# Kernel tuning notes

Hardware: AMD Instinct MI355X
Metric: run time of the kernel (lower is better)

Reference implementation:

```python
import jax, jax.numpy as jnp
import numpy as np

D_MODEL = 512
D_INNER = 1024   # expand * d_model
D_STATE = 16
DT_RANK = 32     # ceil(d_model / 16)
D_CONV = 4
BATCH = 4
SEQLEN = 2304
DILATIONS = (1, 2, 4)


def _dw(x, w, pad, dil=1):
    # depthwise 1D conv: x (B,C,L), w (C,1,K)
    return jax.lax.conv_general_dilated(
        x, w, window_strides=(1,), padding=[pad], rhs_dilation=(dil,),
        dimension_numbers=('NCH', 'OIH', 'NCH'), feature_group_count=x.shape[1])


def setup_inputs() -> dict:
    key = jax.random.key(0)
    ks = iter(jax.random.split(key, 32))
    nrm = lambda shape, s=0.02: jax.random.normal(next(ks), shape, jnp.float32) * s
    std = DT_RANK ** -0.5
    return dict(
        hidden_states=jax.random.normal(next(ks), (BATCH, SEQLEN, D_MODEL), jnp.float32),
        in_proj_w=nrm((5 * D_INNER, D_MODEL)),
        conv1d_w=nrm((D_INNER, 1, D_CONV), 0.2),
        conv1d_b=jnp.zeros((D_INNER,), jnp.float32),
        x_proj_w=nrm((DT_RANK + 2 * D_STATE, D_INNER)),
        dt_proj_w=jax.random.uniform(next(ks), (D_INNER, DT_RANK), jnp.float32, -std, std),
        dt_proj_b=jax.random.uniform(next(ks), (D_INNER,), jnp.float32, -5.0, -1.0),
        A_log=jnp.log(jnp.broadcast_to(jnp.arange(1, D_STATE + 1, dtype=jnp.float32), (D_INNER, D_STATE))),
        D=jnp.ones((D_INNER,), jnp.float32),
        out_proj_w=nrm((D_MODEL, 3 * D_INNER)),
        cb_local_w=nrm((D_MODEL, 1, 3), 0.2), cb_local_b=jnp.zeros((D_MODEL,), jnp.float32),
        cb_global_w=nrm((D_MODEL, 1, 1), 0.2), cb_global_b=jnp.zeros((D_MODEL,), jnp.float32),
        cb_pre_w=nrm((3, D_MODEL, 1, 1), 0.2), cb_pre_b=jnp.zeros((3, D_MODEL), jnp.float32),
        cb_dil_w=nrm((3, D_MODEL, 1, 3), 0.2), cb_dil_b=jnp.zeros((3, D_MODEL), jnp.float32),
        cb_ln_g=jnp.ones((4 * D_MODEL,), jnp.float32), cb_ln_b=jnp.zeros((4 * D_MODEL,), jnp.float32),
        cb_fuse_w=nrm((2 * D_MODEL, 4 * D_MODEL, 1)), cb_fuse_b=jnp.zeros((2 * D_MODEL,), jnp.float32),
    )


def reference(hidden_states, in_proj_w, conv1d_w, conv1d_b, x_proj_w, dt_proj_w,
              dt_proj_b, A_log, D, out_proj_w, cb_local_w, cb_local_b,
              cb_global_w, cb_global_b, cb_pre_w, cb_pre_b, cb_dil_w, cb_dil_b,
              cb_ln_g, cb_ln_b, cb_fuse_w, cb_fuse_b):
    B, L, dm = hidden_states.shape
    d_inner = D.shape[0]
    d_state = A_log.shape[1]
    dt_rank = dt_proj_w.shape[1]

    # in_proj -> (B, 5*d_inner, L)
    xz = jnp.einsum('ed,bld->bel', in_proj_w, hidden_states)
    xz_f = xz[:, :2 * d_inner]
    xz_b = xz[:, 2 * d_inner:4 * d_inner]
    xz_1 = xz[:, 4 * d_inner:]
    # bidirectional: stack forward and time-flipped backward along batch
    xzc = jnp.concatenate([xz_f, jnp.flip(xz_b, -1)], axis=0)  # (2B, 2*d_inner, L)
    x, z = xzc[:, :d_inner], xzc[:, d_inner:]

    # causal depthwise conv + SiLU
    kc = conv1d_w.shape[-1]
    x = _dw(x, conv1d_w, (kc - 1, 0)) + conv1d_b[None, :, None]
    x = jax.nn.silu(x)

    # x_proj -> dt, B, C
    x_dbl = jnp.einsum('kd,bdl->bkl', x_proj_w, x)
    dt = x_dbl[:, :dt_rank]
    Bm = x_dbl[:, dt_rank:dt_rank + d_state]
    Cm = x_dbl[:, dt_rank + d_state:]
    delta = jax.nn.softplus(jnp.einsum('dr,brl->bdl', dt_proj_w, dt) + dt_proj_b[None, :, None])
    A = -jnp.exp(A_log)  # (d, n)

    # selective scan over time
    delta_l = jnp.moveaxis(delta, 2, 0)  # (L, 2B, d)
    u_l = jnp.moveaxis(x, 2, 0)          # (L, 2B, d)
    B_l = jnp.moveaxis(Bm, 2, 0)         # (L, 2B, n)
    C_l = jnp.moveaxis(Cm, 2, 0)         # (L, 2B, n)

    def step(h, t):
        dl, ul, Bl, Cl = t
        dA = jnp.exp(dl[..., None] * A)                    # (2B, d, n)
        h = dA * h + (dl * ul)[..., None] * Bl[:, None, :]
        y = jnp.einsum('bdn,bn->bd', h, Cl)
        return h, y

    h0 = jnp.zeros((x.shape[0], d_inner, d_state), x.dtype)
    _, ys = jax.lax.scan(step, h0, (delta_l, u_l, B_l, C_l))
    y = jnp.moveaxis(ys, 0, 2)  # (2B, d, L)
    y = y + D[None, :, None] * x
    y = y * jax.nn.silu(z)
    out = jnp.concatenate([y[:B], jnp.flip(y[B:], -1)], axis=1)  # (B, 2*d_inner, L)

    # ConvBranch on xz_1 (2*dm channels -> split into xa, xc of dm each)
    xa, xc = xz_1[:, :dm], xz_1[:, dm:]
    local = jax.nn.gelu(_dw(xc, cb_local_w, (1, 1)) + cb_local_b[None, :, None], approximate=False)
    phi = jax.nn.relu(cb_global_w[:, 0, 0][None, :] * xc.mean(-1) + cb_global_b[None, :])  # (B, dm)
    feats = []
    for i, d in enumerate(DILATIONS):
        xp = cb_pre_w[i, :, 0, 0][None, :, None] * xa + cb_pre_b[i][None, :, None]
        feats.append(_dw(xp, cb_dil_w[i], (d, d), dil=d) + cb_dil_b[i][None, :, None])
    cat = jnp.concatenate(feats + [phi[:, :, None] * local], axis=1)  # (B, 4*dm, L)
    c = cat.transpose(0, 2, 1)
    mu = c.mean(-1, keepdims=True)
    var = c.var(-1, keepdims=True)
    c = (c - mu) / jnp.sqrt(var + 1e-5) * cb_ln_g + cb_ln_b
    cat = c.transpose(0, 2, 1)
    out_c = jnp.einsum('oc,bcl->bol', cb_fuse_w[:, :, 0], cat) + cb_fuse_b[None, :, None]  # (B, 2*d_inner... = d_inner? no: 2*dm, L)

    out_f = jnp.concatenate([out, out_c], axis=1)  # (B, 3*d_inner, L)
    return jnp.einsum('md,bdl->blm', out_proj_w, out_f)  # (B, L, d_model)
```

## Files before the change

### kernel.cpp

```cpp
#include <hip/hip_runtime.h>
#include <math.h>

#define L 2304
#define NB 4
#define NCH 36
#define STILE 64
#define SPAD 68
#define DLU_PAD 130

typedef __attribute__((ext_vector_type(8))) short short8v;
typedef __attribute__((ext_vector_type(4))) float f32x4;

__device__ inline unsigned short f2bf(float x) {
    unsigned u = __float_as_uint(x);
    return (unsigned short)((u + 0x7fffu + ((u >> 16) & 1u)) >> 16);
}
__device__ inline void split1(float x, unsigned short& h, unsigned short& l) {
    h = f2bf(x);
    float hf = __uint_as_float((unsigned)h << 16);
    l = f2bf(x - hf);
}

__device__ __forceinline__ void gload16(const unsigned short* g, unsigned short* l)
{
    __builtin_amdgcn_global_load_lds(
        (const __attribute__((address_space(1))) unsigned int*)g,
        (__attribute__((address_space(3))) unsigned int*)l, 16, 0, 0);
}

__device__ inline float row_reduce16(float v) {
    v += __int_as_float(__builtin_amdgcn_update_dpp(0, __float_as_int(v), 0xB1, 0xF, 0xF, true));
    v += __int_as_float(__builtin_amdgcn_update_dpp(0, __float_as_int(v), 0x4E, 0xF, 0xF, true));
    v += __int_as_float(__builtin_amdgcn_update_dpp(0, __float_as_int(v), 0x124, 0xF, 0xF, true));
    v += __int_as_float(__builtin_amdgcn_update_dpp(0, __float_as_int(v), 0x128, 0xF, 0xF, true));
    return v;
}

__global__ __launch_bounds__(256) void split_kernel(
    const float* __restrict__ src, unsigned short* __restrict__ hi,
    unsigned short* __restrict__ lo, int n)
{
    int i = (blockIdx.x * 256 + threadIdx.x) * 4;
    if (i >= n) return;
    float4 v = *(const float4*)(src + i);
    unsigned short h0, h1, h2, h3, l0, l1, l2, l3;
    split1(v.x, h0, l0); split1(v.y, h1, l1);
    split1(v.z, h2, l2); split1(v.w, h3, l3);
    ushort4 hv; hv.x = h0; hv.y = h1; hv.z = h2; hv.w = h3;
    ushort4 lv; lv.x = l0; lv.y = l1; lv.z = l2; lv.w = l3;
    *(ushort4*)(hi + i) = hv;
    *(ushort4*)(lo + i) = lv;
}

__global__ __launch_bounds__(256) void split_t_kernel(
    const float* __restrict__ src, unsigned short* __restrict__ hiT,
    unsigned short* __restrict__ loT, int C)
{
    __shared__ float tile[64][65];
    const int l0 = blockIdx.x * 64, c0 = blockIdx.y * 64;
    const int li = threadIdx.x & 63, q = threadIdx.x >> 6;
    for (int cc = q; cc < 64; cc += 4)
        tile[cc][li] = src[(long)(c0 + cc) * L + l0 + li];
    __syncthreads();
    const int ci = threadIdx.x & 63;
    for (int ll = q; ll < 64; ll += 4) {
        float x = tile[ci][ll];
        unsigned short h, l;
        split1(x, h, l);
        long o = (long)(l0 + ll) * C + c0 + ci;
        hiT[o] = h;
        loT[o] = l;
    }
}

__global__ __launch_bounds__(256) void gemm_mfma(
    const unsigned short* __restrict__ Ahi, const unsigned short* __restrict__ Alo, int lda,
    const unsigned short* __restrict__ Bhi, const unsigned short* __restrict__ Blo, int ldb,
    float* __restrict__ C, long cms, long cns, int K, int act,
    const float* __restrict__ emu, const float* __restrict__ ers,
    const float* __restrict__ es1, const float* __restrict__ es2)
{
    __shared__ unsigned short Ah[128 * 32], Al[128 * 32], Bh[128 * 32], Bl[128 * 32];
    const int tid = threadIdx.x;
    const int lane = tid & 63, wave = tid >> 6;
    const int wm = (wave >> 1) * 64, wn = (wave & 1) * 64;
    const int m0 = blockIdx.x * 128, n0 = blockIdx.y * 128;
    const int rowS = tid >> 2;
    const int cS = ((tid & 3) ^ ((tid >> 3) & 3)) * 8;
    const unsigned short* gAh0 = Ahi + (long)(m0 + rowS) * lda + cS;
    const unsigned short* gAl0 = Alo + (long)(m0 + rowS) * lda + cS;
    const unsigned short* gBh0 = Bhi + (long)(n0 + rowS) * ldb + cS;
    const unsigned short* gBl0 = Blo + (long)(n0 + rowS) * ldb + cS;
    const long a64 = (long)64 * lda, b64 = (long)64 * ldb;
    unsigned short* lAh0 = Ah + tid * 8;  unsigned short* lAh1 = Ah + 2048 + tid * 8;
    unsigned short* lAl0 = Al + tid * 8;  unsigned short* lAl1 = Al + 2048 + tid * 8;
    unsigned short* lBh0 = Bh + tid * 8;  unsigned short* lBh1 = Bh + 2048 + tid * 8;
    unsigned short* lBl0 = Bl + tid * 8;  unsigned short* lBl1 = Bl + 2048 + tid * 8;
    const int fr = lane & 15;
    const int chq = (((lane >> 4) ^ ((fr >> 1) & 3)) << 3);

    f32x4 acc[4][4];
#pragma unroll
    for (int i = 0; i < 4; ++i)
#pragma unroll
        for (int j = 0; j < 4; ++j) acc[i][j] = (f32x4){0.f, 0.f, 0.f, 0.f};

    for (int k0 = 0; k0 < K; k0 += 32) {
        gload16(gAh0 + k0, lAh0); gload16(gAh0 + a64 + k0, lAh1);
        gload16(gAl0 + k0, lAl0); gload16(gAl0 + a64 + k0, lAl1);
        gload16(gBh0 + k0, lBh0); gload16(gBh0 + b64 + k0, lBh1);
        gload16(gBl0 + k0, lBl0); gload16(gBl0 + b64 + k0, lBl1);
        __syncthreads();
        short8v bhf[4], blf[4];
#pragma unroll
        for (int nf = 0; nf < 4; ++nf) {
            bhf[nf] = *(const short8v*)&Bh[(wn + nf * 16 + fr) * 32 + chq];
            blf[nf] = *(const short8v*)&Bl[(wn + nf * 16 + fr) * 32 + chq];
        }
#pragma unroll
        for (int mf = 0; mf < 4; ++mf) {
            short8v ah = *(const short8v*)&Ah[(wm + mf * 16 + fr) * 32 + chq];
            short8v al = *(const short8v*)&Al[(wm + mf * 16 + fr) * 32 + chq];
#pragma unroll
            for (int nf = 0; nf < 4; ++nf) {
                acc[mf][nf] = __builtin_amdgcn_mfma_f32_16x16x32_bf16(ah, bhf[nf], acc[mf][nf], 0, 0, 0);
                acc[mf][nf] = __builtin_amdgcn_mfma_f32_16x16x32_bf16(ah, blf[nf], acc[mf][nf], 0, 0, 0);
                acc[mf][nf] = __builtin_amdgcn_mfma_f32_16x16x32_bf16(al, bhf[nf], acc[mf][nf], 0, 0, 0);
            }
        }
        __syncthreads();
    }
    const int rb = (lane >> 4) * 4;
#pragma unroll
    for (int mf = 0; mf < 4; ++mf) {
#pragma unroll
        for (int nf = 0; nf < 4; ++nf) {
            int n = n0 + wn + nf * 16 + fr;
            int mb = m0 + wm + mf * 16 + rb;
            if (cms == 1) {
                float4 r;
                r.x = acc[mf][nf][0]; r.y = acc[mf][nf][1];
                r.z = acc[mf][nf][2]; r.w = acc[mf][nf][3];
                *(float4*)(C + (long)n * cns + mb) = r;
            } else {
#pragma unroll
                for (int r = 0; r < 4; ++r) {
                    int m = mb + r;
                    float v = acc[mf][nf][r];
                    if (act == 2) v = (v - emu[n] * es1[m]) * ers[n] + es2[m];
                    C[(long)m * cms + n] = v;
                }
            }
        }
    }
}

__global__ __launch_bounds__(256) void gemm_mfma128sk(
    const unsigned short* __restrict__ Ahi, const unsigned short* __restrict__ Alo, int lda,
    const unsigned short* __restrict__ Bhi, const unsigned short* __restrict__ Blo, int ldb,
    float* __restrict__ P, int KS, int Mstride)
{
    __shared__ unsigned short Ah[128 * 32], Al[128 * 32], Bh[128 * 32], Bl[128 * 32];
    const int tid = threadIdx.x;
    const int lane = tid & 63, wave = tid >> 6;
    const int wm = (wave >> 1) * 64, wn = (wave & 1) * 64;
    const int nwg = gridDim.x * gridDim.y * gridDim.z;
    const int bid = blockIdx.x + gridDim.x * (blockIdx.y + gridDim.y * blockIdx.z);
    const int cpx = nwg >> 3;
    const int swz = (bid & 7) * cpx + (bid >> 3);
    const int bx = swz % gridDim.x;
    const int rest = swz / gridDim.x;
    const int by = rest % gridDim.y;
    const int sl = rest / gridDim.y;
    const int m0 = bx * 128, n0 = by * 128;
    const int kbase = sl * KS;
    const int rowS = tid >> 2;
    const int cS = ((tid & 3) ^ ((tid >> 3) & 3)) * 8;
    const unsigned short* gAh0 = Ahi + (long)(m0 + rowS) * lda + kbase + cS;
    const unsigned short* gAl0 = Alo + (long)(m0 + rowS) * lda + kbase + cS;
    const unsigned short* gBh0 = Bhi + (long)(n0 + rowS) * ldb + kbase + cS;
    const unsigned short* gBl0 = Blo + (long)(n0 + rowS) * ldb + kbase + cS;
    const long a64 = (long)64 * lda, b64 = (long)64 * ldb;
    unsigned short* lAh0 = Ah + tid * 8;  unsigned short* lAh1 = Ah + 2048 + tid * 8;
    unsigned short* lAl0 = Al + tid * 8;  unsigned short* lAl1 = Al + 2048 + tid * 8;
    unsigned short* lBh0 = Bh + tid * 8;  unsigned short* lBh1 = Bh + 2048 + tid * 8;
    unsigned short* lBl0 = Bl + tid * 8;  unsigned short* lBl1 = Bl + 2048 + tid * 8;
    const int fr = lane & 15;
    const int chq = (((lane >> 4) ^ ((fr >> 1) & 3)) << 3);

    f32x4 acc[4][4];
#pragma unroll
    for (int i = 0; i < 4; ++i)
#pragma unroll
        for (int j = 0; j < 4; ++j) acc[i][j] = (f32x4){0.f, 0.f, 0.f, 0.f};

    for (int k0 = 0; k0 < KS; k0 += 32) {
        gload16(gAh0 + k0, lAh0); gload16(gAh0 + a64 + k0, lAh1);
        gload16(gAl0 + k0, lAl0); gload16(gAl0 + a64 + k0, lAl1);
        gload16(gBh0 + k0, lBh0); gload16(gBh0 + b64 + k0, lBh1);
        gload16(gBl0 + k0, lBl0); gload16(gBl0 + b64 + k0, lBl1);
        __syncthreads();
        short8v bhf[4], blf[4];
#pragma unroll
        for (int nf = 0; nf < 4; ++nf) {
            bhf[nf] = *(const short8v*)&Bh[(wn + nf * 16 + fr) * 32 + chq];
            blf[nf] = *(const short8v*)&Bl[(wn + nf * 16 + fr) * 32 + chq];
        }
#pragma unroll
        for (int mf = 0; mf < 4; ++mf) {
            short8v ah = *(const short8v*)&Ah[(wm + mf * 16 + fr) * 32 + chq];
            short8v al = *(const short8v*)&Al[(wm + mf * 16 + fr) * 32 + chq];
#pragma unroll
            for (int nf = 0; nf < 4; ++nf) {
                acc[mf][nf] = __builtin_amdgcn_mfma_f32_16x16x32_bf16(ah, bhf[nf], acc[mf][nf], 0, 0, 0);
                acc[mf][nf] = __builtin_amdgcn_mfma_f32_16x16x32_bf16(ah, blf[nf], acc[mf][nf], 0, 0, 0);
                acc[mf][nf] = __builtin_amdgcn_mfma_f32_16x16x32_bf16(al, bhf[nf], acc[mf][nf], 0, 0, 0);
            }
        }
        __syncthreads();
    }
    const int rb = (lane >> 4) * 4;
    float* Pp = P + (long)sl * Mstride * L;
#pragma unroll
    for (int mf = 0; mf < 4; ++mf) {
#pragma unroll
        for (int nf = 0; nf < 4; ++nf) {
            int n = n0 + wn + nf * 16 + fr;
            int mb = m0 + wm + mf * 16 + rb;
            float4 r;
            r.x = acc[mf][nf][0]; r.y = acc[mf][nf][1];
            r.z = acc[mf][nf][2]; r.w = acc[mf][nf][3];
            *(float4*)(Pp + (long)n * Mstride + mb) = r;
        }
    }
}

__global__ __launch_bounds__(256) void out_reduce(
    const float* __restrict__ P, float* __restrict__ out)
{
    const long E = (long)512 * L;
    long i = ((long)blockIdx.x * 256 + threadIdx.x) * 4;
    float4 r = *(const float4*)(P + i);
#pragma unroll
    for (int s = 1; s < 8; ++s) {
        float4 a = *(const float4*)(P + (long)s * E + i);
        r.x += a.x; r.y += a.y; r.z += a.z; r.w += a.w;
    }
    *(float4*)(out + i) = r;
}

__global__ __launch_bounds__(256) void fuse_reduce(
    const float* __restrict__ P,
    const float* __restrict__ emu, const float* __restrict__ ers,
    const float* __restrict__ es1, const float* __restrict__ es2,
    float* __restrict__ out)
{
    __shared__ float tile[64][65];
    const int m0 = blockIdx.x * 64, n0 = blockIdx.y * 64;
    const int li = threadIdx.x & 63, q = threadIdx.x >> 6;
    const long E = (long)1024 * L;
    for (int nn = q; nn < 64; nn += 4) {
        long base = (long)(n0 + nn) * 1024 + m0 + li;
        tile[nn][li] = (P[base] + P[E + base]) + (P[2 * E + base] + P[3 * E + base]);
    }
    __syncthreads();
    for (int mm = q; mm < 64; mm += 4) {
        int m = m0 + mm, n = n0 + li;
        float v = tile[li][mm];
        v = (v - emu[n] * es1[m]) * ers[n] + es2[m];
        out[(long)m * L + n] = v;
    }
}

__global__ __launch_bounds__(256) void gemm_f32(
    const float* __restrict__ A, int lda,
    const float* __restrict__ B, long ldb, int b_nk, long bbs,
    float* __restrict__ C, long cms, long cns, long cbs,
    int M, int N, int K,
    const float* __restrict__ bias, int act,
    const float* __restrict__ emu, const float* __restrict__ ers,
    const float* __restrict__ es1, const float* __restrict__ es2)
{
    __shared__ float As[16][65];
    __shared__ float Bs[16][65];
    const int tid = threadIdx.x;
    const int tx = tid & 15, ty = tid >> 4;
    const int m0 = blockIdx.x * 64, n0 = blockIdx.y * 64;
    const int bz = blockIdx.z;
    const float* Bb = B + (long)bz * bbs;
    float acc[4][4];
#pragma unroll
    for (int i = 0; i < 4; ++i)
#pragma unroll
        for (int j = 0; j < 4; ++j) acc[i][j] = 0.f;

    for (int k0 = 0; k0 < K; k0 += 16) {
        {
            int m = tid >> 2, kq = (tid & 3) << 2;
            float4 v = *(const float4*)(A + (long)(m0 + m) * lda + (k0 + kq));
            As[kq + 0][m] = v.x; As[kq + 1][m] = v.y; As[kq + 2][m] = v.z; As[kq + 3][m] = v.w;
        }
        if (b_nk) {
            int n = tid >> 2, kq = (tid & 3) << 2;
            float4 v = *(const float4*)(Bb + (long)(n0 + n) * ldb + (k0 + kq));
            Bs[kq + 0][n] = v.x; Bs[kq + 1][n] = v.y; Bs[kq + 2][n] = v.z; Bs[kq + 3][n] = v.w;
        } else {
            int k = tid >> 4, nq = (tid & 15) << 2;
            float4 v = *(const float4*)(Bb + (long)(k0 + k) * ldb + (n0 + nq));
            Bs[k][nq + 0] = v.x; Bs[k][nq + 1] = v.y; Bs[k][nq + 2] = v.z; Bs[k][nq + 3] = v.w;
        }
        __syncthreads();
#pragma unroll
        for (int kk = 0; kk < 16; ++kk) {
            float a[4], b[4];
#pragma unroll
            for (int i = 0; i < 4; ++i) a[i] = As[kk][ty * 4 + i];
#pragma unroll
            for (int j = 0; j < 4; ++j) b[j] = Bs[kk][tx * 4 + j];
#pragma unroll
            for (int i = 0; i < 4; ++i)
#pragma unroll
                for (int j = 0; j < 4; ++j) acc[i][j] = fmaf(a[i], b[j], acc[i][j]);
        }
        __syncthreads();
    }
#pragma unroll
    for (int i = 0; i < 4; ++i) {
        int m = m0 + ty * 4 + i;
        float bs = bias ? bias[m] : 0.f;
        float s1 = es1 ? es1[m] : 0.f;
        float s2 = es2 ? es2[m] : 0.f;
#pragma unroll
        for (int j = 0; j < 4; ++j) {
            int n = n0 + tx * 4 + j;
            float v = acc[i][j] + bs;
            if (act == 1) v = (v > 20.f) ? v : log1pf(expf(v));
            else if (act == 2) {
                float mu = emu[n];
                float rs = ers[n];
                v = (v - mu * s1) * rs + s2;
            }
            C[(long)bz * cbs + (long)m * cms + (long)n * cns] = v;
        }
    }
}

__global__ __launch_bounds__(256) void xproj_partial(
    const float* __restrict__ W, const float* __restrict__ xconv,
    float* __restrict__ P)
{
    __shared__ float As[16][65];
    __shared__ float Bs[16][65];
    const int tid = threadIdx.x;
    const int tx = tid & 15, ty = tid >> 4;
    const int n0 = blockIdx.x * 64;
    const int dir = blockIdx.y, sl = blockIdx.z;
    const float* A = W + sl * 256;
    const float* B = xconv + ((long)dir * 1024 + sl * 256) * L;
    float* Pp = P + ((long)sl * 2 + dir) * 64 * L;
    float acc[4][4];
#pragma unroll
    for (int i = 0; i < 4; ++i)
#pragma unroll
        for (int j = 0; j < 4; ++j) acc[i][j] = 0.f;

    for (int k0 = 0; k0 < 256; k0 += 16) {
        {
            int m = tid >> 2, kq = (tid & 3) << 2;
            float4 v = *(const float4*)(A + (long)m * 1024 + (k0 + kq));
            As[kq + 0][m] = v.x; As[kq + 1][m] = v.y; As[kq + 2][m] = v.z; As[kq + 3][m] = v.w;
        }
        {
            int k = tid >> 4, nq = (tid & 15) << 2;
            float4 v = *(const float4*)(B + (long)(k0 + k) * L + (n0 + nq));
            Bs[k][nq + 0] = v.x; Bs[k][nq + 1] = v.y; Bs[k][nq + 2] = v.z; Bs[k][nq + 3] = v.w;
        }
        __syncthreads();
#pragma unroll
        for (int kk = 0; kk < 16; ++kk) {
            float a[4], b[4];
#pragma unroll
            for (int i = 0; i < 4; ++i) a[i] = As[kk][ty * 4 + i];
#pragma unroll
            for (int j = 0; j < 4; ++j) b[j] = Bs[kk][tx * 4 + j];
#pragma unroll
            for (int i = 0; i < 4; ++i)
#pragma unroll
                for (int j = 0; j < 4; ++j) acc[i][j] = fmaf(a[i], b[j], acc[i][j]);
        }
        __syncthreads();
    }
#pragma unroll
    for (int i = 0; i < 4; ++i) {
        int m = ty * 4 + i;
        float4 r;
        r.x = acc[i][0]; r.y = acc[i][1]; r.z = acc[i][2]; r.w = acc[i][3];
        *(float4*)(Pp + (long)m * L + n0 + tx * 4) = r;
    }
}

__global__ __launch_bounds__(256) void xproj_reduce(
    const float* __restrict__ P, float* __restrict__ xdbl)
{
    const long E = (long)2 * 64 * L;
    long i = ((long)blockIdx.x * 256 + threadIdx.x) * 4;
    float4 a = *(const float4*)(P + i);
    float4 b = *(const float4*)(P + E + i);
    float4 c = *(const float4*)(P + 2 * E + i);
    float4 d = *(const float4*)(P + 3 * E + i);
    float4 r;
    r.x = (a.x + b.x) + (c.x + d.x);
    r.y = (a.y + b.y) + (c.y + d.y);
    r.z = (a.z + b.z) + (c.z + d.z);
    r.w = (a.w + b.w) + (c.w + d.w);
    *(float4*)(xdbl + i) = r;
}

__global__ __launch_bounds__(256) void mamba_conv_kernel(
    const float* __restrict__ xz_b, const float* __restrict__ w,
    const float* __restrict__ bias, float* __restrict__ xout)
{
    long idx = (long)blockIdx.x * 256 + threadIdx.x;
    int l = (int)(idx % L);
    long r = idx / L;
    int d = (int)(r % 1024);
    int dir = (int)(r / 1024);
    const float* src = xz_b + ((dir ? 2048 : 0) + (long)d) * L;
    float acc = bias[d];
#pragma unroll
    for (int j = 0; j < 4; ++j) {
        int t = l - 3 + j;
        if (t >= 0) {
            float v = dir ? src[L - 1 - t] : src[t];
            acc = fmaf(w[d * 4 + j], v, acc);
        }
    }
    xout[idx] = acc / (1.f + expf(-acc));
}

__global__ __launch_bounds__(256) void scan_pass1(
    const float* __restrict__ delta_b, const float* __restrict__ xconv_b,
    const float* __restrict__ xdbl_b, const float* __restrict__ A_log,
    float* __restrict__ hend, float* __restrict__ pAb)
{
    __shared__ float s_dlu[16][DLU_PAD];
    __shared__ float s_B[16][SPAD];
    const int tid = threadIdx.x;
    const int dir = blockIdx.y, ch = blockIdx.z;
    const int n = tid & 15, dloc = tid >> 4;
    const int d0 = blockIdx.x * 16;
    const int d = d0 + dloc;
    const int t0 = ch * STILE;
    const float Adn = -expf(A_log[d * 16 + n]);
    const float* dl_p = delta_b + ((long)dir * 1024 + d0) * L;
    const float* u_p  = xconv_b + ((long)dir * 1024 + d0) * L;
    const float* B_p  = xdbl_b + ((long)dir * 64 + 32) * L;
    const int lch = tid >> 4, lq = tid & 15;
    {
        float4 a = *(const float4*)(dl_p + (long)lch * L + t0 + lq * 4);
        float4 b = *(const float4*)(u_p + (long)lch * L + t0 + lq * 4);
        float4 w0; w0.x = a.x; w0.y = b.x; w0.z = a.y; w0.w = b.y;
        float4 w1; w1.x = a.z; w1.y = b.z; w1.z = a.w; w1.w = b.w;
        *(float4*)&s_dlu[lch][lq * 8] = w0;
        *(float4*)&s_dlu[lch][lq * 8 + 4] = w1;
        float4 v = *(const float4*)(B_p + (long)lch * L + t0 + lq * 4);
        *(float4*)&s_B[lch][lq * 4] = v;
    }
    __syncthreads();
    float h = 0.f, p = 1.f;
#pragma unroll 4
    for (int tt = 0; tt < STILE; ++tt) {
        float2 dlu = *(const float2*)&s_dlu[dloc][tt * 2];
        float Bv = s_B[n][tt];
        float dA = __expf(dlu.x * Adn);
        h = fmaf(dA, h, dlu.x * dlu.y * Bv);
        p *= dA;
    }
    long sidx = (((long)dir * NCH + ch) * 1024 + d) * 16 + n;
    hend[sidx] = h;
    pAb[sidx] = p;
}

__global__ __launch_bounds__(256) void scan_fix(
    const float* __restrict__ hend, const float* __restrict__ pAb,
    float* __restrict__ hin)
{
    int tid = blockIdx.x * 256 + threadIdx.x;
    int dir = tid >> 14;
    int rest = tid & 16383;
    float h = 0.f;
#pragma unroll
    for (int c = 0; c < NCH; ++c) {
        long idx = (((long)dir * NCH + c) << 14) + rest;
        hin[idx] = h;
        h = hend[idx] + pAb[idx] * h;
    }
}

__global__ __launch_bounds__(256) void scan_pass2(
    const float* __restrict__ delta_b, const float* __restrict__ xconv_b,
    const float* __restrict__ xdbl_b, const float* __restrict__ xz_b,
    const float* __restrict__ A_log, const float* __restrict__ Dvec,
    const float* __restrict__ hin, float* __restrict__ out_fb)
{
    __shared__ float s_dlu[16][DLU_PAD];
    __shared__ float s_BC[16][DLU_PAD];
    const int tid = threadIdx.x;
    const int dir = blockIdx.y, ch = blockIdx.z;
    const int n = tid & 15, dloc = tid >> 4;
    const int d0 = blockIdx.x * 16;
    const int d = d0 + dloc;
    const int t0 = ch * STILE;
    const int opos0 = dir ? (L - STILE - t0) : t0;
    const float Adn = -expf(A_log[d * 16 + n]);
    const float Dd = Dvec[d];
    const float* dl_p = delta_b + ((long)dir * 1024 + d0) * L;
    const float* u_p  = xconv_b + ((long)dir * 1024 + d0) * L;
    const float* B_p  = xdbl_b + ((long)dir * 64 + 32) * L;
    const float* C_p  = xdbl_b + ((long)dir * 64 + 48) * L;
    const float* z_p  = xz_b + ((dir ? 3072 : 1024) + (long)d0) * L;
    float* o_p = out_fb + ((dir ? 1024 : 0) + (long)d0) * L;
    const int lch = tid >> 4, lq = tid & 15;
    {
        float4 a = *(const float4*)(dl_p + (long)lch * L + t0 + lq * 4);
        float4 b = *(const float4*)(u_p + (long)lch * L + t0 + lq * 4);
        float4 w0; w0.x = a.x; w0.y = b.x; w0.z = a.y; w0.w = b.y;
        float4 w1; w1.x = a.z; w1.y = b.z; w1.z = a.w; w1.w = b.w;
        *(float4*)&s_dlu[lch][lq * 8] = w0;
        *(float4*)&s_dlu[lch][lq * 8 + 4] = w1;
        float4 c = *(const float4*)(B_p + (long)lch * L + t0 + lq * 4);
        float4 e = *(const float4*)(C_p + (long)lch * L + t0 + lq * 4);
        float4 x0; x0.x = c.x; x0.y = e.x; x0.z = c.y; x0.w = e.y;
        float4 x1; x1.x = c.z; x1.y = e.z; x1.z = c.w; x1.w = e.w;
        *(float4*)&s_BC[lch][lq * 8] = x0;
        *(float4*)&s_BC[lch][lq * 8 + 4] = x1;
    }
    __syncthreads();
    float h = hin[(((long)dir * NCH + ch) * 1024 + d) * 16 + n];
#pragma unroll 4
    for (int tt = 0; tt < STILE; ++tt) {
        float2 dlu = *(const float2*)&s_dlu[dloc][tt * 2];
        float2 bc = *(const float2*)&s_BC[n][tt * 2];
        float dA = __expf(dlu.x * Adn);
        h = fmaf(dA, h, dlu.x * dlu.y * bc.x);
        float y = row_reduce16(h * bc.y);
        if (n == 0) s_dlu[dloc][tt * 2] = y + Dd * dlu.y;
    }
    {
        float* po = o_p + (long)lch * L + opos0;
        const float* pz = z_p + (long)lch * L + opos0;
        int oo = lq * 4;
        float4 zv = *(const float4*)(pz + oo);
        float y0 = s_dlu[lch][(dir ? 63 - oo : oo) * 2];
        float y1 = s_dlu[lch][(dir ? 62 - oo : oo + 1) * 2];
        float y2 = s_dlu[lch][(dir ? 61 - oo : oo + 2) * 2];
        float y3 = s_dlu[lch][(dir ? 60 - oo : oo + 3) * 2];
        float4 r;
        r.x = y0 * (zv.x / (1.f + __expf(-zv.x)));
        r.y = y1 * (zv.y / (1.f + __expf(-zv.y)));
        r.z = y2 * (zv.z / (1.f + __expf(-zv.z)));
        r.w = y3 * (zv.w / (1.f + __expf(-zv.w)));
        *(float4*)(po + oo) = r;
    }
}

__global__ __launch_bounds__(256) void mean_phi_kernel(
    const float* __restrict__ xz_b, const float* __restrict__ gw,
    const float* __restrict__ gb, float* __restrict__ phi_b)
{
    int c = blockIdx.x;
    const float* src = xz_b + (4608 + (long)c) * L;
    float s = 0.f;
    for (int l = threadIdx.x; l < L; l += 256) s += src[l];
    __shared__ float red[256];
    red[threadIdx.x] = s;
    __syncthreads();
    for (int st = 128; st > 0; st >>= 1) {
        if (threadIdx.x < st) red[threadIdx.x] += red[threadIdx.x + st];
        __syncthreads();
    }
    if (threadIdx.x == 0) {
        float m = red[0] / (float)L;
        phi_b[c] = fmaxf(gw[c] * m + gb[c], 0.f);
    }
}

__global__ __launch_bounds__(256) void cat_build_kernel(
    const float* __restrict__ xz_b,
    const float* __restrict__ lw, const float* __restrict__ lb,
    const float* __restrict__ pw, const float* __restrict__ pb,
    const float* __restrict__ dw, const float* __restrict__ db,
    const float* __restrict__ phi_b, float* __restrict__ cat_b)
{
    long idx = (long)blockIdx.x * 256 + threadIdx.x;
    int l = (int)(idx % L);
    int cc = (int)(idx / L);
    float val;
    if (cc < 1536) {
        int i = cc >> 9, c = cc & 511, dil = 1 << i;
        const float* xa = xz_b + (4096 + (long)c) * L;
        float pwv = pw[i * 512 + c], pbv = pb[i * 512 + c];
        const float* w = dw + ((long)i * 512 + c) * 3;
        float acc = db[i * 512 + c];
#pragma unroll
        for (int k = 0; k < 3; ++k) {
            int t = l + (k - 1) * dil;
            if (t >= 0 && t < L) acc += (pwv * xa[t] + pbv) * w[k];
        }
        val = acc;
    } else {
        int c = cc & 511;
        const float* xc = xz_b + (4608 + (long)c) * L;
        float acc = lb[c];
#pragma unroll
        for (int k = 0; k < 3; ++k) {
            int t = l - 1 + k;
            if (t >= 0 && t < L) acc += xc[t] * lw[c * 3 + k];
        }
        float g = 0.5f * acc * (1.f + erff(acc * 0.70710678118f));
        val = phi_b[c] * g;
    }
    cat_b[idx] = val;
}

__global__ __launch_bounds__(256) void ln_partial_kernel(
    const float* __restrict__ cat_b, float* __restrict__ ps, float* __restrict__ pq)
{
    int l = blockIdx.x * 256 + threadIdx.x;
    int g = blockIdx.y;
    const float* p = cat_b + (long)g * 64 * L + l;
    float s = 0.f, q = 0.f;
#pragma unroll 8
    for (int c = 0; c < 64; ++c) {
        float v = p[(long)c * L];
        s += v;
        q = fmaf(v, v, q);
    }
    ps[g * L + l] = s;
    pq[g * L + l] = q;
}

__global__ __launch_bounds__(256) void ln_final_kernel(
    const float* __restrict__ ps, const float* __restrict__ pq,
    float* __restrict__ mu_b, float* __restrict__ rsig_b)
{
    int l = blockIdx.x * 256 + threadIdx.x;
    float s = 0.f, q = 0.f;
#pragma unroll
    for (int g = 0; g < 32; ++g) {
        s += ps[g * L + l];
        q += pq[g * L + l];
    }
    float m = s * (1.f / 2048.f);
    float var = q * (1.f / 2048.f) - m * m;
    mu_b[l] = m;
    rsig_b[l] = rsqrtf(var + 1e-5f);
}

__global__ __launch_bounds__(256) void ln_stats_kernel(
    const float* __restrict__ cat_b, float* __restrict__ mu_b, float* __restrict__ rsig_b)
{
    int tx = threadIdx.x & 63, ty = threadIdx.x >> 6;
    int l = blockIdx.x * 64 + tx;
    float s = 0.f, s2 = 0.f;
    for (int c = ty; c < 2048; c += 4) {
        float v = cat_b[(long)c * L + l];
        s += v;
        s2 += v * v;
    }
    __shared__ float rs[4][64], rq[4][64];
    rs[ty][tx] = s;
    rq[ty][tx] = s2;
    __syncthreads();
    if (ty == 0) {
        float S = rs[0][tx] + rs[1][tx] + rs[2][tx] + rs[3][tx];
        float Q = rq[0][tx] + rq[1][tx] + rq[2][tx] + rq[3][tx];
        float m = S * (1.f / 2048.f);
        float var = Q * (1.f / 2048.f) - m * m;
        mu_b[l] = m;
        rsig_b[l] = rsqrtf(var + 1e-5f);
    }
}

__global__ __launch_bounds__(256) void fuse_pre_kernel(
    const float* __restrict__ fw, const float* __restrict__ g,
    const float* __restrict__ lbn, const float* __restrict__ fb,
    float* __restrict__ wg, float* __restrict__ S1, float* __restrict__ S2)
{
    int o = blockIdx.x;
    float s1 = 0.f, s2 = 0.f;
    for (int c = threadIdx.x; c < 2048; c += 256) {
        float w = fw[(long)o * 2048 + c];
        float v = w * g[c];
        wg[(long)o * 2048 + c] = v;
        s1 += v;
        s2 += w * lbn[c];
    }
    __shared__ float r1[256], r2[256];
    r1[threadIdx.x] = s1;
    r2[threadIdx.x] = s2;
    __syncthreads();
    for (int st = 128; st > 0; st >>= 1) {
        if (threadIdx.x < st) {
            r1[threadIdx.x] += r1[threadIdx.x + st];
            r2[threadIdx.x] += r2[threadIdx.x + st];
        }
        __syncthreads();
    }
    if (threadIdx.x == 0) {
        S1[o] = r1[0];
        S2[o] = r2[0] + fb[o];
    }
}

__global__ __launch_bounds__(256) void fuse_pre_split_kernel(
    const float* __restrict__ fw, const float* __restrict__ g,
    const float* __restrict__ lbn, const float* __restrict__ fb,
    unsigned short* __restrict__ wg_hi, unsigned short* __restrict__ wg_lo,
    float* __restrict__ S1, float* __restrict__ S2)
{
    int o = blockIdx.x;
    float s1 = 0.f, s2 = 0.f;
    for (int c = threadIdx.x; c < 2048; c += 256) {
        float w = fw[(long)o * 2048 + c];
        float v = w * g[c];
        unsigned short h, l;
        split1(v, h, l);
        wg_hi[(long)o * 2048 + c] = h;
        wg_lo[(long)o * 2048 + c] = l;
        s1 += v;
        s2 += w * lbn[c];
    }
    __shared__ float r1[256], r2[256];
    r1[threadIdx.x] = s1;
    r2[threadIdx.x] = s2;
    __syncthreads();
    for (int st = 128; st > 0; st >>= 1) {
        if (threadIdx.x < st) {
            r1[threadIdx.x] += r1[threadIdx.x + st];
            r2[threadIdx.x] += r2[threadIdx.x + st];
        }
        __syncthreads();
    }
    if (threadIdx.x == 0) {
        S1[o] = r1[0];
        S2[o] = r2[0] + fb[o];
    }
}

extern "C" void kernel_launch(void* const* d_in, const int* in_sizes, int n_in,
                              void* d_out, int out_size, void* d_ws, size_t ws_size,
                              hipStream_t stream)
{
    const float* hidden     = (const float*)d_in[0];
    const float* in_proj_w  = (const float*)d_in[1];
    const float* conv1d_w   = (const float*)d_in[2];
    const float* conv1d_b   = (const float*)d_in[3];
    const float* x_proj_w   = (const float*)d_in[4];
    const float* dt_proj_w  = (const float*)d_in[5];
    const float* dt_proj_b  = (const float*)d_in[6];
    const float* A_log      = (const float*)d_in[7];
    const float* Dvec       = (const float*)d_in[8];
    const float* out_proj_w = (const float*)d_in[9];
    const float* cb_local_w = (const float*)d_in[10];
    const float* cb_local_b = (const float*)d_in[11];
    const float* cb_global_w= (const float*)d_in[12];
    const float* cb_global_b= (const float*)d_in[13];
    const float* cb_pre_w   = (const float*)d_in[14];
    const float* cb_pre_b   = (const float*)d_in[15];
    const float* cb_dil_w   = (const float*)d_in[16];
    const float* cb_dil_b   = (const float*)d_in[17];
    const float* cb_ln_g    = (const float*)d_in[18];
    const float* cb_ln_b    = (const float*)d_in[19];
    const float* cb_fuse_w  = (const float*)d_in[20];
    const float* cb_fuse_b  = (const float*)d_in[21];

    float* ws = (float*)d_ws;
    const size_t CSZ = (size_t)2 * NCH * 1024 * 16;

    size_t off = 0;
    float* S1    = ws + off; off += 1024;
    float* S2    = ws + off; off += 1024;
    float* xz_b  = ws + off; off += (size_t)5120 * L;
    float* out_fb= ws + off; off += (size_t)3072 * L;
    float* cat_b = ws + off; off += (size_t)2048 * L;
    float* delta_b = cat_b;
    float* xconv_b = ws + off; off += (size_t)2048 * L;
    float* xdbl_b  = ws + off; off += (size_t)128 * L;
    float* mu_b    = ws + off; off += L;
    float* rsig_b  = ws + off; off += L;
    float* phi_b   = ws + off; off += 512;
    float* lnps    = ws + off; off += (size_t)32 * L;
    float* lnpq    = ws + off; off += (size_t)32 * L;
    float* hend = ws + off; off += CSZ;
    float* pAb  = ws + off; off += CSZ;
    float* hin  = ws + off; off += CSZ;
    unsigned short* wg_hi  = (unsigned short*)(ws + off); off += (size_t)1024 * 2048 / 2;
    unsigned short* wg_lo  = (unsigned short*)(ws + off); off += (size_t)1024 * 2048 / 2;
    unsigned short* inW_hi = (unsigned short*)(ws + off); off += (size_t)5120 * 512 / 2;
    unsigned short* inW_lo = (unsigned short*)(ws + off); off += (size_t)5120 * 512 / 2;
    unsigned short* outW_hi= (unsigned short*)(ws + off); off += (size_t)512 * 3072 / 2;
    unsigned short* outW_lo= (unsigned short*)(ws + off); off += (size_t)512 * 3072 / 2;
    unsigned short* BT_hi  = (unsigned short*)(ws + off); off += (size_t)3072 * L / 2;
    unsigned short* BT_lo  = (unsigned short*)(ws + off); off += (size_t)3072 * L / 2;
    size_t need_mfma = off * sizeof(float);

    float* xpP = out_fb;
    float* fsP = cat_b;
    float* opP = cat_b;

    if (ws_size >= need_mfma) {
        fuse_pre_split_kernel<<<1024, 256, 0, stream>>>(
            cb_fuse_w, cb_ln_g, cb_ln_b, cb_fuse_b, wg_hi, wg_lo, S1, S2);
        split_kernel<<<(5120 * 512) / 1024, 256, 0, stream>>>(in_proj_w, inW_hi, inW_lo, 5120 * 512);
        split_kernel<<<(512 * 3072) / 1024, 256, 0, stream>>>(out_proj_w, outW_hi, outW_lo, 512 * 3072);

        for (int b = 0; b < NB; ++b) {
            const float* hid_b = hidden + (size_t)b * L * 512;
            float* out_b = (float*)d_out + (size_t)b * L * 512;

            split_kernel<<<(L * 512) / 1024, 256, 0, stream>>>(hid_b, BT_hi, BT_lo, L * 512);
            gemm_mfma<<<dim3(5120 / 128, L / 128), 256, 0, stream>>>(
                inW_hi, inW_lo, 512, BT_hi, BT_lo, 512,
                xz_b, L, 1, 512, 0, nullptr, nullptr, nullptr, nullptr);

            mean_phi_kernel<<<512, 256, 0, stream>>>(xz_b, cb_global_w, cb_global_b, phi_b);
            cat_build_kernel<<<(2048 * L) / 256, 256, 0, stream>>>(
                xz_b, cb_local_w, cb_local_b, cb_pre_w, cb_pre_b, cb_dil_w, cb_dil_b, phi_b, cat_b);
            ln_partial_kernel<<<dim3(L / 256, 32), 256, 0, stream>>>(cat_b, lnps, lnpq);
            ln_final_kernel<<<L / 256, 256, 0, stream>>>(lnps, lnpq, mu_b, rsig_b);
            split_t_kernel<<<dim3(L / 64, 2048 / 64), 256, 0, stream>>>(cat_b, BT_hi, BT_lo, 2048);
            gemm_mfma128sk<<<dim3(1024 / 128, L / 128, 4), 256, 0, stream>>>(
                wg_hi, wg_lo, 2048, BT_hi, BT_lo, 2048, fsP, 512, 1024);
            fuse_reduce<<<dim3(1024 / 64, L / 64), 256, 0, stream>>>(
                fsP, mu_b, rsig_b, S1, S2, out_fb + (long)2048 * L);

            mamba_conv_kernel<<<(2 * 1024 * L) / 256, 256, 0, stream>>>(
                xz_b, conv1d_w, conv1d_b, xconv_b);
            xproj_partial<<<dim3(L / 64, 2, 4), 256, 0, stream>>>(
                x_proj_w, xconv_b, xpP);
            xproj_reduce<<<(2 * 64 * L / 4) / 256, 256, 0, stream>>>(xpP, xdbl_b);
            gemm_f32<<<dim3(1024 / 64, L / 64, 2), 256, 0, stream>>>(
                dt_proj_w, 32, xdbl_b, L, 0, (long)64 * L,
                delta_b, L, 1, (long)1024 * L, 1024, L, 32,
                dt_proj_b, 1, nullptr, nullptr, nullptr, nullptr);
            scan_pass1<<<dim3(64, 2, NCH), 256, 0, stream>>>(
                delta_b, xconv_b, xdbl_b, A_log, hend, pAb);
            scan_fix<<<128, 256, 0, stream>>>(hend, pAb, hin);
            scan_pass2<<<dim3(64, 2, NCH), 256, 0, stream>>>(
                delta_b, xconv_b, xdbl_b, xz_b, A_log, Dvec, hin, out_fb);

            split_t_kernel<<<dim3(L / 64, 3072 / 64), 256, 0, stream>>>(out_fb, BT_hi, BT_lo, 3072);
            gemm_mfma128sk<<<dim3(512 / 128, L / 128, 8), 256, 0, stream>>>(
                outW_hi, outW_lo, 3072, BT_hi, BT_lo, 3072, opP, 384, 512);
            out_reduce<<<(512 * L / 4) / 256, 256, 0, stream>>>(opP, out_b);
        }
        return;
    }

    off = 0;
    float* wg    = ws + off; off += (size_t)1024 * 2048;
    S1    = ws + off; off += 1024;
    S2    = ws + off; off += 1024;
    xz_b  = ws + off; off += (size_t)5120 * L;
    out_fb= ws + off; off += (size_t)3072 * L;
    cat_b = ws + off; off += (size_t)2048 * L;
    delta_b = cat_b;
    xconv_b = ws + off; off += (size_t)2048 * L;
    xdbl_b  = ws + off; off += (size_t)128 * L;
    mu_b    = ws + off; off += L;
    rsig_b  = ws + off; off += L;
    phi_b   = ws + off; off += 512;
    hend = ws + off; off += CSZ;
    pAb  = ws + off; off += CSZ;
    hin  = ws + off; off += CSZ;
    if (ws_size < off * sizeof(float)) return;

    fuse_pre_kernel<<<1024, 256, 0, stream>>>(cb_fuse_w, cb_ln_g, cb_ln_b, cb_fuse_b, wg, S1, S2);

    for (int b = 0; b < NB; ++b) {
        const float* hid_b = hidden + (size_t)b * L * 512;
        float* out_b = (float*)d_out + (size_t)b * L * 512;

        gemm_f32<<<dim3(5120 / 64, L / 64, 1), 256, 0, stream>>>(
            in_proj_w, 512, hid_b, 512, 1, 0,
            xz_b, L, 1, 0, 5120, L, 512,
            nullptr, 0, nullptr, nullptr, nullptr, nullptr);

        mean_phi_kernel<<<512, 256, 0, stream>>>(xz_b, cb_global_w, cb_global_b, phi_b);
        cat_build_kernel<<<(2048 * L) / 256, 256, 0, stream>>>(
            xz_b, cb_local_w, cb_local_b, cb_pre_w, cb_pre_b, cb_dil_w, cb_dil_b, phi_b, cat_b);
        ln_stats_kernel<<<L / 64, 256, 0, stream>>>(cat_b, mu_b, rsig_b);
        gemm_f32<<<dim3(1024 / 64, L / 64, 1), 256, 0, stream>>>(
            wg, 2048, cat_b, L, 0, 0,
            out_fb + (long)2048 * L, L, 1, 0, 1024, L, 2048,
            nullptr, 2, mu_b, rsig_b, S1, S2);

        mamba_conv_kernel<<<(2 * 1024 * L) / 256, 256, 0, stream>>>(
            xz_b, conv1d_w, conv1d_b, xconv_b);
        gemm_f32<<<dim3(1, L / 64, 2), 256, 0, stream>>>(
            x_proj_w, 1024, xconv_b, L, 0, (long)1024 * L,
            xdbl_b, L, 1, (long)64 * L, 64, L, 1024,
            nullptr, 0, nullptr, nullptr, nullptr, nullptr);
        gemm_f32<<<dim3(1024 / 64, L / 64, 2), 256, 0, stream>>>(
            dt_proj_w, 32, xdbl_b, L, 0, (long)64 * L,
            delta_b, L, 1, (long)1024 * L, 1024, L, 32,
            dt_proj_b, 1, nullptr, nullptr, nullptr, nullptr);
        scan_pass1<<<dim3(64, 2, NCH), 256, 0, stream>>>(
            delta_b, xconv_b, xdbl_b, A_log, hend, pAb);
        scan_fix<<<128, 256, 0, stream>>>(hend, pAb, hin);
        scan_pass2<<<dim3(64, 2, NCH), 256, 0, stream>>>(
            delta_b, xconv_b, xdbl_b, xz_b, A_log, Dvec, hin, out_fb);

        gemm_f32<<<dim3(512 / 64, L / 64, 1), 256, 0, stream>>>(
            out_proj_w, 3072, out_fb, L, 0, 0,
            out_b, 1, 512, 0, 512, L, 3072,
            nullptr, 0, nullptr, nullptr, nullptr, nullptr);
    }
}
```

Baseline: 1.282 ms.

## Fuse bf16 hi/lo split and transpose into fuse_reduce and scan_pass2 epilogues

fuse_reduce and scan_pass2 now write their results directly as transposed bf16 hi/lo pairs into the B operand buffer of the output-projection GEMM. This removes the fp32 out_fb round trip and the separate split_t_kernel pass over the 3072xL activation. In exchange, the scan epilogue stores become 8-byte writes strided by 3072 elements, so they are less coalesced than before. fuse_reduce also changes from a shared-memory tile transpose to a flat float4 reduction.

```diff
diff --git a/kernel.cpp b/kernel.cpp
--- a/kernel.cpp
+++ b/kernel.cpp
@@ -249,27 +249,39 @@
     *(float4*)(out + i) = r;
 }
 
-__global__ __launch_bounds__(256) void fuse_reduce(
+__global__ __launch_bounds__(256) void fuse_reduce_bt(
     const float* __restrict__ P,
     const float* __restrict__ emu, const float* __restrict__ ers,
     const float* __restrict__ es1, const float* __restrict__ es2,
-    float* __restrict__ out)
-{
-    __shared__ float tile[64][65];
-    const int m0 = blockIdx.x * 64, n0 = blockIdx.y * 64;
-    const int li = threadIdx.x & 63, q = threadIdx.x >> 6;
+    unsigned short* __restrict__ BT_hi, unsigned short* __restrict__ BT_lo)
+{
     const long E = (long)1024 * L;
-    for (int nn = q; nn < 64; nn += 4) {
-        long base = (long)(n0 + nn) * 1024 + m0 + li;
-        tile[nn][li] = (P[base] + P[E + base]) + (P[2 * E + base] + P[3 * E + base]);
-    }
-    __syncthreads();
-    for (int mm = q; mm < 64; mm += 4) {
-        int m = m0 + mm, n = n0 + li;
-        float v = tile[li][mm];
-        v = (v - emu[n] * es1[m]) * ers[n] + es2[m];
-        out[(long)m * L + n] = v;
-    }
+    long idx = (long)blockIdx.x * 256 + threadIdx.x;
+    int l = (int)(idx >> 8);
+    int dq = (int)(idx & 255) * 4;
+    long base = (long)l * 1024 + dq;
+    float4 a = *(const float4*)(P + base);
+    float4 b = *(const float4*)(P + E + base);
+    float4 c = *(const float4*)(P + 2 * E + base);
+    float4 d = *(const float4*)(P + 3 * E + base);
+    float v[4];
+    v[0] = (a.x + b.x) + (c.x + d.x);
+    v[1] = (a.y + b.y) + (c.y + d.y);
+    v[2] = (a.z + b.z) + (c.z + d.z);
+    v[3] = (a.w + b.w) + (c.w + d.w);
+    float mu = emu[l], rs = ers[l];
+    unsigned short hv[4], lv[4];
+#pragma unroll
+    for (int j = 0; j < 4; ++j) {
+        int m = dq + j;
+        float x = (v[j] - mu * es1[m]) * rs + es2[m];
+        split1(x, hv[j], lv[j]);
+    }
+    long o = (long)l * 3072 + 2048 + dq;
+    ushort4 h4; h4.x = hv[0]; h4.y = hv[1]; h4.z = hv[2]; h4.w = hv[3];
+    ushort4 l4; l4.x = lv[0]; l4.y = lv[1]; l4.z = lv[2]; l4.w = lv[3];
+    *(ushort4*)(BT_hi + o) = h4;
+    *(ushort4*)(BT_lo + o) = l4;
 }
 
 __global__ __launch_bounds__(256) void gemm_f32(
@@ -494,6 +506,79 @@
         long idx = (((long)dir * NCH + c) << 14) + rest;
         hin[idx] = h;
         h = hend[idx] + pAb[idx] * h;
+    }
+}
+
+__global__ __launch_bounds__(256) void scan_pass2_bt(
+    const float* __restrict__ delta_b, const float* __restrict__ xconv_b,
+    const float* __restrict__ xdbl_b, const float* __restrict__ xz_b,
+    const float* __restrict__ A_log, const float* __restrict__ Dvec,
+    const float* __restrict__ hin,
+    unsigned short* __restrict__ BT_hi, unsigned short* __restrict__ BT_lo)
+{
+    __shared__ float s_dlu[16][DLU_PAD];
+    __shared__ float s_BC[16][DLU_PAD];
+    const int tid = threadIdx.x;
+    const int dir = blockIdx.y, ch = blockIdx.z;
+    const int n = tid & 15, dloc = tid >> 4;
+    const int d0 = blockIdx.x * 16;
+    const int d = d0 + dloc;
+    const int t0 = ch * STILE;
+    const int opos0 = dir ? (L - STILE - t0) : t0;
+    const float Adn = -expf(A_log[d * 16 + n]);
+    const float Dd = Dvec[d];
+    const float* dl_p = delta_b + ((long)dir * 1024 + d0) * L;
+    const float* u_p  = xconv_b + ((long)dir * 1024 + d0) * L;
+    const float* B_p  = xdbl_b + ((long)dir * 64 + 32) * L;
+    const float* C_p  = xdbl_b + ((long)dir * 64 + 48) * L;
+    const float* z_base = xz_b + ((dir ? 3072 : 1024) + (long)d0) * L;
+    const int lch = tid >> 4, lq = tid & 15;
+    {
+        float4 a = *(const float4*)(dl_p + (long)lch * L + t0 + lq * 4);
+        float4 b = *(const float4*)(u_p + (long)lch * L + t0 + lq * 4);
+        float4 w0; w0.x = a.x; w0.y = b.x; w0.z = a.y; w0.w = b.y;
+        float4 w1; w1.x = a.z; w1.y = b.z; w1.z = a.w; w1.w = b.w;
+        *(float4*)&s_dlu[lch][lq * 8] = w0;
+        *(float4*)&s_dlu[lch][lq * 8 + 4] = w1;
+        float4 c = *(const float4*)(B_p + (long)lch * L + t0 + lq * 4);
+        float4 e = *(const float4*)(C_p + (long)lch * L + t0 + lq * 4);
+        float4 x0; x0.x = c.x; x0.y = e.x; x0.z = c.y; x0.w = e.y;
+        float4 x1; x1.x = c.z; x1.y = e.z; x1.z = c.w; x1.w = e.w;
+        *(float4*)&s_BC[lch][lq * 8] = x0;
+        *(float4*)&s_BC[lch][lq * 8 + 4] = x1;
+    }
+    __syncthreads();
+    float h = hin[(((long)dir * NCH + ch) * 1024 + d) * 16 + n];
+#pragma unroll 4
+    for (int tt = 0; tt < STILE; ++tt) {
+        float2 dlu = *(const float2*)&s_dlu[dloc][tt * 2];
+        float2 bc = *(const float2*)&s_BC[n][tt * 2];
+        float dA = __expf(dlu.x * Adn);
+        h = fmaf(dA, h, dlu.x * dlu.y * bc.x);
+        float y = row_reduce16(h * bc.y);
+        if (n == 0) s_dlu[dloc][tt * 2] = y + Dd * dlu.y;
+    }
+    __syncthreads();
+    {
+        const int p = tid >> 2;
+        const int dq = (tid & 3) * 4;
+        const int l = opos0 + p;
+        const int cbase = (dir ? 1024 : 0) + d0;
+        const int yi = (dir ? 63 - p : p) * 2;
+        unsigned short hv[4], lv[4];
+#pragma unroll
+        for (int j = 0; j < 4; ++j) {
+            int dl = dq + j;
+            float y = s_dlu[dl][yi];
+            float z = z_base[(long)dl * L + l];
+            float v = y * (z / (1.f + __expf(-z)));
+            split1(v, hv[j], lv[j]);
+        }
+        long o = (long)l * 3072 + cbase + dq;
+        ushort4 h4; h4.x = hv[0]; h4.y = hv[1]; h4.z = hv[2]; h4.w = hv[3];
+        ushort4 l4; l4.x = lv[0]; l4.y = lv[1]; l4.z = lv[2]; l4.w = lv[3];
+        *(ushort4*)(BT_hi + o) = h4;
+        *(ushort4*)(BT_lo + o) = l4;
     }
 }
 
@@ -832,8 +917,8 @@
             split_t_kernel<<<dim3(L / 64, 2048 / 64), 256, 0, stream>>>(cat_b, BT_hi, BT_lo, 2048);
             gemm_mfma128sk<<<dim3(1024 / 128, L / 128, 4), 256, 0, stream>>>(
                 wg_hi, wg_lo, 2048, BT_hi, BT_lo, 2048, fsP, 512, 1024);
-            fuse_reduce<<<dim3(1024 / 64, L / 64), 256, 0, stream>>>(
-                fsP, mu_b, rsig_b, S1, S2, out_fb + (long)2048 * L);
+            fuse_reduce_bt<<<L, 256, 0, stream>>>(
+                fsP, mu_b, rsig_b, S1, S2, BT_hi, BT_lo);
 
             mamba_conv_kernel<<<(2 * 1024 * L) / 256, 256, 0, stream>>>(
                 xz_b, conv1d_w, conv1d_b, xconv_b);
@@ -847,10 +932,9 @@
             scan_pass1<<<dim3(64, 2, NCH), 256, 0, stream>>>(
                 delta_b, xconv_b, xdbl_b, A_log, hend, pAb);
             scan_fix<<<128, 256, 0, stream>>>(hend, pAb, hin);
-            scan_pass2<<<dim3(64, 2, NCH), 256, 0, stream>>>(
-                delta_b, xconv_b, xdbl_b, xz_b, A_log, Dvec, hin, out_fb);
-
-            split_t_kernel<<<dim3(L / 64, 3072 / 64), 256, 0, stream>>>(out_fb, BT_hi, BT_lo, 3072);
+            scan_pass2_bt<<<dim3(64, 2, NCH), 256, 0, stream>>>(
+                delta_b, xconv_b, xdbl_b, xz_b, A_log, Dvec, hin, BT_hi, BT_lo);
+
             gemm_mfma128sk<<<dim3(512 / 128, L / 128, 8), 256, 0, stream>>>(
                 outW_hi, outW_lo, 3072, BT_hi, BT_lo, 3072, opP, 384, 512);
             out_reduce<<<(512 * L / 4) / 256, 256, 0, stream>>>(opP, out_b);
```

After: 1.237 ms (median of 2 runs). 1.04x faster.
